# Kernel tuning notes

Hardware: AMD Instinct MI355X
Metric: run time of the kernel (lower is better)

The kernel has to match this reference:

```python
import jax, jax.numpy as jnp
import numpy as np
import math

B, L, C = 4096, 64, 256   # L == window_size
H = 8                     # num_heads
META_H = 384


def _rel_coords_log(W):
    # coords = meshgrid(arange(1), arange(W)) -> (2, W); first row is zeros
    c0 = jnp.zeros((W,), jnp.float32)
    c1 = jnp.arange(W, dtype=jnp.float32)
    coords = jnp.stack([c0, c1], axis=0)                      # (2, W)
    rel = coords[:, :, None] - coords[:, None, :]             # (2, W, W)
    rel = rel.transpose(1, 2, 0).reshape(-1, 2)               # (W*W, 2)
    return jnp.sign(rel) * jnp.log1p(jnp.abs(rel))


def setup_inputs() -> dict:
    key = jax.random.key(0)
    ks = jax.random.split(key, 8)
    s = 0.02
    return {
        "x": jax.random.normal(ks[0], (B, L, C), jnp.float32),
        "qkv_w": jax.random.normal(ks[1], (3 * C, C), jnp.float32) * s,
        "qkv_b": jnp.zeros((3 * C,), jnp.float32),
        "proj_w": jax.random.normal(ks[2], (C, C), jnp.float32) * s,
        "proj_b": jnp.zeros((C,), jnp.float32),
        "logit_scale": jnp.full((H,), math.log(10.0), jnp.float32),
        "mlp1_w": jax.random.normal(ks[3], (META_H, 2), jnp.float32) * s,
        "mlp1_b": jnp.zeros((META_H,), jnp.float32),
        "mlp2_w": jax.random.normal(ks[4], (H, META_H), jnp.float32) * s,
        "mlp2_b": jnp.zeros((H,), jnp.float32),
    }


def reference(x, qkv_w, qkv_b, proj_w, proj_b, logit_scale, mlp1_w, mlp1_b, mlp2_w, mlp2_b):
    b, l, c = x.shape
    h = H
    d = c // h
    qkv = x @ qkv_w.T + qkv_b                                 # (B, L, 3C)
    qkv = qkv.reshape(b, l, 3, h, d).transpose(2, 0, 3, 1, 4) # (3, B, H, L, D)
    q, k, v = qkv[0], qkv[1], qkv[2]
    # cosine attention: L2-normalize q, k (F.normalize, eps=1e-12)
    qn = q / jnp.maximum(jnp.linalg.norm(q, axis=-1, keepdims=True), 1e-12)
    kn = k / jnp.maximum(jnp.linalg.norm(k, axis=-1, keepdims=True), 1e-12)
    attn = jnp.einsum("bhld,bhmd->bhlm", qn, kn)              # (B, H, L, L)
    scale = jnp.exp(jnp.minimum(logit_scale, math.log(1.0 / 0.01)))
    attn = attn * scale.reshape(1, h, 1, 1)
    # MLP relative position bias
    rel = _rel_coords_log(l)                                  # (L*L, 2)
    hid = jax.nn.relu(rel @ mlp1_w.T + mlp1_b)                # (L*L, META_H)
    bias = (hid @ mlp2_w.T + mlp2_b).T.reshape(h, l, l)       # (H, L, L)
    attn = jax.nn.softmax(attn + bias[None], axis=-1)
    out = jnp.einsum("bhlm,bhmd->bhld", attn, v)              # (B, H, L, D)
    out = out.transpose(0, 2, 1, 3).reshape(b, l, c)
    return out @ proj_w.T + proj_b
```

## Files before the change

kernel.cpp:

```cpp
#include <hip/hip_runtime.h>
#include <hip/hip_bf16.h>

typedef __attribute__((ext_vector_type(4))) float f32x4;
typedef __attribute__((ext_vector_type(8))) short short8;
typedef __attribute__((ext_vector_type(4))) short short4_t;

#define LTOK 64
#define CDIM 256
#define FRS 576

static __device__ __forceinline__ short f2bf(float f) {
    __hip_bfloat16 h = __float2bfloat16(f);
    union { __hip_bfloat16 b; short s; } u; u.b = h;
    return u.s;
}
static __device__ __forceinline__ float bf2f(short s) {
    union { unsigned u; float f; } v;
    v.u = ((unsigned)(unsigned short)s) << 16;
    return v.f;
}
static __device__ __forceinline__ int KL(int l) { return l + (l >> 3); }

__global__ void prep_all(const float* __restrict__ qw, const float* __restrict__ pw,
                         const float* __restrict__ w1, const float* __restrict__ b1,
                         const float* __restrict__ w2, const float* __restrict__ b2,
                         const float* __restrict__ lsc,
                         short* __restrict__ wqs, short* __restrict__ wps,
                         float* __restrict__ biasT, float* __restrict__ scT) {
    if (blockIdx.x == 768) {
        int t = threadIdx.x;
        if (t < 8) scT[t] = expf(fminf(lsc[t], logf(100.0f)));
        if (t < 127) {
            float delta = (float)(t - 63);
            float sg = (delta > 0.f) ? 1.f : ((delta < 0.f) ? -1.f : 0.f);
            float r = sg * log1pf(fabsf(delta));
            float acc[8];
            #pragma unroll
            for (int q = 0; q < 8; ++q) acc[q] = b2[q];
            for (int m = 0; m < 384; ++m) {
                float hid = fmaxf(fmaf(r, w1[m * 2 + 1], b1[m]), 0.f);
                #pragma unroll
                for (int q = 0; q < 8; ++q) acc[q] = fmaf(hid, w2[q * 384 + m], acc[q]);
            }
            #pragma unroll
            for (int q = 0; q < 8; ++q) biasT[q * 127 + t] = acc[q];
        }
        return;
    }
    int i = blockIdx.x * 256 + threadIdx.x;
    {
        int row = i >> 8, col = i & 255;
        int nt = row >> 4, lcr = row & 15;
        int kt = col >> 5, lg = (col >> 3) & 3, j = col & 7;
        wqs[(size_t)(((nt * 8 + kt) * 64) + lg * 16 + lcr) * 8 + j] = f2bf(qw[i]);
    }
    if (i < 256 * 256) {
        int row = i >> 8, col = i & 255;
        int gs = row >> 4, lcr = row & 15;
        int h = col >> 5, lg = (col >> 3) & 3, j = col & 7;
        wps[(size_t)(((gs * 8 + h) * 64) + lg * 16 + lcr) * 8 + j] = f2bf(pw[i]);
    }
}


__global__ void __launch_bounds__(256, 5)
fused_win_attn(const float* __restrict__ x,
               const float* __restrict__ qkv_b,
               const short* __restrict__ wqs,
               const float* __restrict__ biasT,
               const float* __restrict__ scT,
               float* out)
{
    __shared__ short SH[13824];

    const int tid = threadIdx.x;
    const int w  = tid >> 6;
    const int l  = tid & 63;
    const int lg = l >> 4;
    const int lc = l & 15;
    const int li4 = lg * 4;
    const int blk = blockIdx.x;
    const int klb = KL(l) * 8;

    short* QGF = SH;
    short* KGF = SH + 4608;
    short* VTF = SH + 9216;

    short* ao = (short*)(out + (size_t)blk * (LTOK * CDIM) + 8192);

    short8 xf[8];
    {
        const float* xr = x + (size_t)blk * (LTOK * CDIM) + (size_t)(w * 16 + lc) * CDIM + lg * 8;
        #pragma unroll
        for (int kt = 0; kt < 8; ++kt) {
            f32x4 a = *(const f32x4*)(xr + kt * 32);
            f32x4 b = *(const f32x4*)(xr + kt * 32 + 4);
            short8 t;
            t[0]=f2bf(a[0]); t[1]=f2bf(a[1]); t[2]=f2bf(a[2]); t[3]=f2bf(a[3]);
            t[4]=f2bf(b[0]); t[5]=f2bf(b[1]); t[6]=f2bf(b[2]); t[7]=f2bf(b[3]);
            xf[kt] = t;
        }
    }
    const f32x4 fzero = {0.f, 0.f, 0.f, 0.f};
    short8 ones;
    #pragma unroll
    for (int j = 0; j < 8; ++j) ones[j] = (short)0x3F80;

    #pragma unroll 1
    for (int g = 0; g < 4; ++g) {
        #pragma unroll
        for (int sg = 0; sg < 6; ++sg) {
            const int st0 = sg * 2, st1 = sg * 2 + 1;
            const int gnt0 = (st0 >> 2) * 16 + g * 4 + (st0 & 3);
            const int gnt1 = (st1 >> 2) * 16 + g * 4 + (st1 & 3);
            const short* wb0 = wqs + ((size_t)(gnt0 * 8) * 64 + l) * 8;
            const short* wb1 = wqs + ((size_t)(gnt1 * 8) * 64 + l) * 8;
            f32x4 a0 = fzero, a1 = fzero;
            #pragma unroll
            for (int kt = 0; kt < 8; ++kt) {
                short8 Bf0 = *(const short8*)(wb0 + kt * 512);
                short8 Bf1 = *(const short8*)(wb1 + kt * 512);
                a0 = __builtin_amdgcn_mfma_f32_16x16x32_bf16(xf[kt], Bf0, a0, 0, 0, 0);
                a1 = __builtin_amdgcn_mfma_f32_16x16x32_bf16(xf[kt], Bf1, a1, 0, 0, 0);
            }
            #pragma unroll
            for (int e = 0; e < 2; ++e) {
                const int strip = e ? st1 : st0;
                const f32x4 av = e ? a1 : a0;
                const int s = strip >> 2, nt = strip & 3;
                const float bq = qkv_b[s * 256 + g * 64 + nt * 16 + lc];
                if (s < 2) {
                    short* base = (s ? KGF : QGF) + ((nt >> 1) * 4 + w) * FRS;
                    const int lgc = (nt & 1) * 2 + (lc >> 3);
                    #pragma unroll
                    for (int i = 0; i < 4; ++i) {
                        const int l2 = lgc * 16 + li4 + i;
                        base[KL(l2) * 8 + (lc & 7)] = f2bf(av[i] + bq);
                    }
                } else {
                    short* base = VTF + ((w >> 1) * 4 + nt) * FRS;
                    const int l2 = ((w & 1) * 2 + (lg >> 1)) * 16 + lc;
                    short4_t pk;
                    #pragma unroll
                    for (int i = 0; i < 4; ++i) pk[i] = f2bf(av[i] + bq);
                    *(short4_t*)(base + KL(l2) * 8 + (li4 & 7)) = pk;
                }
            }
        }
        __syncthreads();

        short8 Aq0 = *(const short8*)(QGF + (0 * 4 + w) * FRS + klb);
        short8 Aq1 = *(const short8*)(QGF + (1 * 4 + w) * FRS + klb);
        short* PW = QGF + w * FRS;

        #pragma unroll 1
        for (int hh = 0; hh < 2; ++hh) {
            const int h = 2 * g + hh;
            const float sc = scT[h];
            const short8 Aq = hh ? Aq1 : Aq0;
            float qn = 1e-24f;
            #pragma unroll
            for (int j = 0; j < 8; ++j) { float v = bf2f(Aq[j]); qn = fmaf(v, v, qn); }
            qn += __shfl_xor(qn, 16);
            qn += __shfl_xor(qn, 32);
            const float rq = rsqrtf(qn);
            f32x4 pacc[4];
            float invk[4];
            #pragma unroll
            for (int nt = 0; nt < 4; ++nt) {
                short8 Bk = *(const short8*)(KGF + (hh * 4 + nt) * FRS + klb);
                pacc[nt] = __builtin_amdgcn_mfma_f32_16x16x32_bf16(Aq, Bk, fzero, 0, 0, 0);
                float kn = 1e-24f;
                #pragma unroll
                for (int j = 0; j < 8; ++j) { float v = bf2f(Bk[j]); kn = fmaf(v, v, kn); }
                kn += __shfl_xor(kn, 16);
                kn += __shfl_xor(kn, 32);
                invk[nt] = rsqrtf(kn);
            }
            float iq[4];
            #pragma unroll
            for (int i = 0; i < 4; ++i) iq[i] = __shfl(rq, li4 + i, 16) * sc;
            const float* bt = biasT + h * 127 + w * 16 + 63 - lc;
            float p[4][4];
            #pragma unroll
            for (int i = 0; i < 4; ++i)
                #pragma unroll
                for (int nt = 0; nt < 4; ++nt)
                    p[i][nt] = __expf(pacc[nt][i] * iq[i] * invk[nt] + bt[li4 + i - nt * 16]);
            #pragma unroll
            for (int i = 0; i < 4; ++i)
                #pragma unroll
                for (int nt = 0; nt < 4; ++nt) {
                    const int l2 = ((nt & 1) * 2 + (lc >> 3)) * 16 + li4 + i;
                    PW[(nt >> 1) * 4 * FRS + KL(l2) * 8 + (lc & 7)] = f2bf(p[i][nt]);
                }
            f32x4 oacc[2], sacc;
            oacc[0] = fzero; oacc[1] = fzero; sacc = fzero;
            #pragma unroll
            for (int ktp = 0; ktp < 2; ++ktp) {
                short8 Ap = *(const short8*)(PW + ktp * 4 * FRS + klb);
                #pragma unroll
                for (int ndv = 0; ndv < 2; ++ndv) {
                    short8 Bv = *(const short8*)(VTF + (ktp * 4 + hh * 2 + ndv) * FRS + klb);
                    oacc[ndv] = __builtin_amdgcn_mfma_f32_16x16x32_bf16(Ap, Bv, oacc[ndv], 0, 0, 0);
                }
                sacc = __builtin_amdgcn_mfma_f32_16x16x32_bf16(Ap, ones, sacc, 0, 0, 0);
            }
            short8 aov;
            #pragma unroll
            for (int ndv = 0; ndv < 2; ++ndv)
                #pragma unroll
                for (int i = 0; i < 4; ++i)
                    aov[ndv * 4 + i] = f2bf(oacc[ndv][i] * (1.f / sacc[i]));
            *(short8*)(ao + ((size_t)((h * 4 + w) * 64 + l)) * 8) = aov;
        }
        __syncthreads();
    }
}

__global__ void __launch_bounds__(256, 4)
proj_win(const float* __restrict__ proj_b,
         const short* __restrict__ wps,
         float* out)
{
    __shared__ short AF[32 * FRS];

    const int tid = threadIdx.x;
    const int w  = tid >> 6;
    const int l  = tid & 63;
    const int lg = l >> 4;
    const int lc = l & 15;
    const int li4 = lg * 4;
    const int blk = blockIdx.x;
    const int klb = KL(l) * 8;

    const short* ao = (const short*)(out + (size_t)blk * (LTOK * CDIM) + 8192);

    #pragma unroll
    for (int u = 0; u < 8; ++u) {
        const int f = w * 8 + u;
        short8 t = *(const short8*)(ao + ((size_t)(f * 64 + l)) * 8);
        #pragma unroll
        for (int j = 0; j < 8; ++j) {
            const int r = lg * 4 + (j & 3);
            const int c = (j >> 2) * 16 + lc;
            AF[f * FRS + KL((c >> 3) * 16 + r) * 8 + (c & 7)] = t[j];
        }
    }
    __syncthreads();

    f32x4 accP[4][4];
    #pragma unroll
    for (int a = 0; a < 4; ++a)
        #pragma unroll
        for (int b = 0; b < 4; ++b) accP[a][b] = (f32x4){0,0,0,0};

    #pragma unroll
    for (int kt = 0; kt < 8; ++kt) {
        short8 Aa0 = *(const short8*)(AF + (kt * 4 + 0) * FRS + klb);
        short8 Aa1 = *(const short8*)(AF + (kt * 4 + 1) * FRS + klb);
        short8 Aa2 = *(const short8*)(AF + (kt * 4 + 2) * FRS + klb);
        short8 Aa3 = *(const short8*)(AF + (kt * 4 + 3) * FRS + klb);
        #pragma unroll
        for (int ntl = 0; ntl < 4; ++ntl) {
            short8 Bp = *(const short8*)(wps + ((size_t)((w * 4 + ntl) * 8 + kt) * 64 + l) * 8);
            accP[0][ntl] = __builtin_amdgcn_mfma_f32_16x16x32_bf16(Aa0, Bp, accP[0][ntl], 0, 0, 0);
            accP[1][ntl] = __builtin_amdgcn_mfma_f32_16x16x32_bf16(Aa1, Bp, accP[1][ntl], 0, 0, 0);
            accP[2][ntl] = __builtin_amdgcn_mfma_f32_16x16x32_bf16(Aa2, Bp, accP[2][ntl], 0, 0, 0);
            accP[3][ntl] = __builtin_amdgcn_mfma_f32_16x16x32_bf16(Aa3, Bp, accP[3][ntl], 0, 0, 0);
        }
    }

    float* ob = out + (size_t)blk * (LTOK * CDIM);
    #pragma unroll
    for (int ntl = 0; ntl < 4; ++ntl) {
        const float pb = proj_b[w * 64 + ntl * 16 + lc];
        #pragma unroll
        for (int mt = 0; mt < 4; ++mt)
            #pragma unroll
            for (int i = 0; i < 4; ++i)
                ob[(size_t)(mt * 16 + li4 + i) * 256 + w * 64 + ntl * 16 + lc] = accP[mt][ntl][i] + pb;
    }
}

extern "C" void kernel_launch(void* const* d_in, const int* in_sizes, int n_in,
                              void* d_out, int out_size, void* d_ws, size_t ws_size,
                              hipStream_t stream) {
    const float* x     = (const float*)d_in[0];
    const float* qkvw  = (const float*)d_in[1];
    const float* qkvb  = (const float*)d_in[2];
    const float* projw = (const float*)d_in[3];
    const float* projb = (const float*)d_in[4];
    const float* lsc   = (const float*)d_in[5];
    const float* w1    = (const float*)d_in[6];
    const float* b1    = (const float*)d_in[7];
    const float* w2    = (const float*)d_in[8];
    const float* b2    = (const float*)d_in[9];
    float* out = (float*)d_out;

    short* wqs   = (short*)d_ws;
    short* wps   = (short*)((char*)d_ws + 393216);
    float* biasT = (float*)((char*)d_ws + 524288);
    float* scT   = (float*)((char*)d_ws + 528384);

    const int nwin = in_sizes[0] / (LTOK * CDIM);

    prep_all<<<769, 256, 0, stream>>>(qkvw, projw, w1, b1, w2, b2, lsc, wqs, wps, biasT, scT);
    fused_win_attn<<<nwin, 256, 0, stream>>>(x, qkvb, wqs, biasT, scT, out);
    proj_win<<<nwin, 256, 0, stream>>>(projb, wps, out);
}
```

Measured before the change: 505.2 us.

## Interleave two heads' QK phase and halve proj LDS for higher occupancy

In the attention kernel the per-head loop is unrolled. Both heads' norms and QK MFMAs are issued together, which raises instruction-level parallelism but holds more registers. The projection kernel now stages the attention output into LDS in two halves using half the shared memory, with an extra barrier, and raises launch bounds from 4 to 5 blocks per CU. This trades an extra sync and register pressure for more resident blocks.

```diff
diff --git a/kernel.cpp b/kernel.cpp
--- a/kernel.cpp
+++ b/kernel.cpp
@@ -153,40 +153,50 @@
         short8 Aq1 = *(const short8*)(QGF + (1 * 4 + w) * FRS + klb);
         short* PW = QGF + w * FRS;
 
-        #pragma unroll 1
-        for (int hh = 0; hh < 2; ++hh) {
-            const int h = 2 * g + hh;
-            const float sc = scT[h];
-            const short8 Aq = hh ? Aq1 : Aq0;
-            float qn = 1e-24f;
-            #pragma unroll
-            for (int j = 0; j < 8; ++j) { float v = bf2f(Aq[j]); qn = fmaf(v, v, qn); }
-            qn += __shfl_xor(qn, 16);
-            qn += __shfl_xor(qn, 32);
-            const float rq = rsqrtf(qn);
-            f32x4 pacc[4];
-            float invk[4];
-            #pragma unroll
-            for (int nt = 0; nt < 4; ++nt) {
-                short8 Bk = *(const short8*)(KGF + (hh * 4 + nt) * FRS + klb);
-                pacc[nt] = __builtin_amdgcn_mfma_f32_16x16x32_bf16(Aq, Bk, fzero, 0, 0, 0);
-                float kn = 1e-24f;
-                #pragma unroll
-                for (int j = 0; j < 8; ++j) { float v = bf2f(Bk[j]); kn = fmaf(v, v, kn); }
-                kn += __shfl_xor(kn, 16);
-                kn += __shfl_xor(kn, 32);
-                invk[nt] = rsqrtf(kn);
-            }
-            float iq[4];
-            #pragma unroll
-            for (int i = 0; i < 4; ++i) iq[i] = __shfl(rq, li4 + i, 16) * sc;
-            const float* bt = biasT + h * 127 + w * 16 + 63 - lc;
+        float qn0 = 1e-24f, qn1 = 1e-24f;
+        #pragma unroll
+        for (int j = 0; j < 8; ++j) {
+            float v0 = bf2f(Aq0[j]); qn0 = fmaf(v0, v0, qn0);
+            float v1 = bf2f(Aq1[j]); qn1 = fmaf(v1, v1, qn1);
+        }
+        qn0 += __shfl_xor(qn0, 16); qn1 += __shfl_xor(qn1, 16);
+        qn0 += __shfl_xor(qn0, 32); qn1 += __shfl_xor(qn1, 32);
+        const float rq0 = rsqrtf(qn0), rq1 = rsqrtf(qn1);
+        const float sc0 = scT[2 * g], sc1 = scT[2 * g + 1];
+        float iq0[4], iq1[4];
+        #pragma unroll
+        for (int i = 0; i < 4; ++i) {
+            iq0[i] = __shfl(rq0, li4 + i, 16) * sc0;
+            iq1[i] = __shfl(rq1, li4 + i, 16) * sc1;
+        }
+        f32x4 pacc0[4], pacc1[4];
+        float invk0[4], invk1[4];
+        #pragma unroll
+        for (int nt = 0; nt < 4; ++nt) {
+            short8 Bk0 = *(const short8*)(KGF + nt * FRS + klb);
+            short8 Bk1 = *(const short8*)(KGF + (4 + nt) * FRS + klb);
+            pacc0[nt] = __builtin_amdgcn_mfma_f32_16x16x32_bf16(Aq0, Bk0, fzero, 0, 0, 0);
+            pacc1[nt] = __builtin_amdgcn_mfma_f32_16x16x32_bf16(Aq1, Bk1, fzero, 0, 0, 0);
+            float kn0 = 1e-24f, kn1 = 1e-24f;
+            #pragma unroll
+            for (int j = 0; j < 8; ++j) {
+                float v0 = bf2f(Bk0[j]); kn0 = fmaf(v0, v0, kn0);
+                float v1 = bf2f(Bk1[j]); kn1 = fmaf(v1, v1, kn1);
+            }
+            kn0 += __shfl_xor(kn0, 16); kn1 += __shfl_xor(kn1, 16);
+            kn0 += __shfl_xor(kn0, 32); kn1 += __shfl_xor(kn1, 32);
+            invk0[nt] = rsqrtf(kn0);
+            invk1[nt] = rsqrtf(kn1);
+        }
+
+        {
+            const float* bt = biasT + (2 * g) * 127 + w * 16 + 63 - lc;
             float p[4][4];
             #pragma unroll
             for (int i = 0; i < 4; ++i)
                 #pragma unroll
                 for (int nt = 0; nt < 4; ++nt)
-                    p[i][nt] = __expf(pacc[nt][i] * iq[i] * invk[nt] + bt[li4 + i - nt * 16]);
+                    p[i][nt] = __expf(pacc0[nt][i] * iq0[i] * invk0[nt] + bt[li4 + i - nt * 16]);
             #pragma unroll
             for (int i = 0; i < 4; ++i)
                 #pragma unroll
@@ -201,7 +211,7 @@
                 short8 Ap = *(const short8*)(PW + ktp * 4 * FRS + klb);
                 #pragma unroll
                 for (int ndv = 0; ndv < 2; ++ndv) {
-                    short8 Bv = *(const short8*)(VTF + (ktp * 4 + hh * 2 + ndv) * FRS + klb);
+                    short8 Bv = *(const short8*)(VTF + (ktp * 4 + ndv) * FRS + klb);
                     oacc[ndv] = __builtin_amdgcn_mfma_f32_16x16x32_bf16(Ap, Bv, oacc[ndv], 0, 0, 0);
                 }
                 sacc = __builtin_amdgcn_mfma_f32_16x16x32_bf16(Ap, ones, sacc, 0, 0, 0);
@@ -212,18 +222,53 @@
                 #pragma unroll
                 for (int i = 0; i < 4; ++i)
                     aov[ndv * 4 + i] = f2bf(oacc[ndv][i] * (1.f / sacc[i]));
-            *(short8*)(ao + ((size_t)((h * 4 + w) * 64 + l)) * 8) = aov;
+            *(short8*)(ao + ((size_t)(((2 * g) * 4 + w) * 64 + l)) * 8) = aov;
+        }
+        {
+            const float* bt = biasT + (2 * g + 1) * 127 + w * 16 + 63 - lc;
+            float p[4][4];
+            #pragma unroll
+            for (int i = 0; i < 4; ++i)
+                #pragma unroll
+                for (int nt = 0; nt < 4; ++nt)
+                    p[i][nt] = __expf(pacc1[nt][i] * iq1[i] * invk1[nt] + bt[li4 + i - nt * 16]);
+            #pragma unroll
+            for (int i = 0; i < 4; ++i)
+                #pragma unroll
+                for (int nt = 0; nt < 4; ++nt) {
+                    const int l2 = ((nt & 1) * 2 + (lc >> 3)) * 16 + li4 + i;
+                    PW[(nt >> 1) * 4 * FRS + KL(l2) * 8 + (lc & 7)] = f2bf(p[i][nt]);
+                }
+            f32x4 oacc[2], sacc;
+            oacc[0] = fzero; oacc[1] = fzero; sacc = fzero;
+            #pragma unroll
+            for (int ktp = 0; ktp < 2; ++ktp) {
+                short8 Ap = *(const short8*)(PW + ktp * 4 * FRS + klb);
+                #pragma unroll
+                for (int ndv = 0; ndv < 2; ++ndv) {
+                    short8 Bv = *(const short8*)(VTF + (ktp * 4 + 2 + ndv) * FRS + klb);
+                    oacc[ndv] = __builtin_amdgcn_mfma_f32_16x16x32_bf16(Ap, Bv, oacc[ndv], 0, 0, 0);
+                }
+                sacc = __builtin_amdgcn_mfma_f32_16x16x32_bf16(Ap, ones, sacc, 0, 0, 0);
+            }
+            short8 aov;
+            #pragma unroll
+            for (int ndv = 0; ndv < 2; ++ndv)
+                #pragma unroll
+                for (int i = 0; i < 4; ++i)
+                    aov[ndv * 4 + i] = f2bf(oacc[ndv][i] * (1.f / sacc[i]));
+            *(short8*)(ao + ((size_t)(((2 * g + 1) * 4 + w) * 64 + l)) * 8) = aov;
         }
         __syncthreads();
     }
 }
 
-__global__ void __launch_bounds__(256, 4)
+__global__ void __launch_bounds__(256, 5)
 proj_win(const float* __restrict__ proj_b,
          const short* __restrict__ wps,
          float* out)
 {
-    __shared__ short AF[32 * FRS];
+    __shared__ short AF[16 * FRS];
 
     const int tid = threadIdx.x;
     const int w  = tid >> 6;
@@ -236,19 +281,6 @@
 
     const short* ao = (const short*)(out + (size_t)blk * (LTOK * CDIM) + 8192);
 
-    #pragma unroll
-    for (int u = 0; u < 8; ++u) {
-        const int f = w * 8 + u;
-        short8 t = *(const short8*)(ao + ((size_t)(f * 64 + l)) * 8);
-        #pragma unroll
-        for (int j = 0; j < 8; ++j) {
-            const int r = lg * 4 + (j & 3);
-            const int c = (j >> 2) * 16 + lc;
-            AF[f * FRS + KL((c >> 3) * 16 + r) * 8 + (c & 7)] = t[j];
-        }
-    }
-    __syncthreads();
-
     f32x4 accP[4][4];
     #pragma unroll
     for (int a = 0; a < 4; ++a)
@@ -256,18 +288,35 @@
         for (int b = 0; b < 4; ++b) accP[a][b] = (f32x4){0,0,0,0};
 
     #pragma unroll
-    for (int kt = 0; kt < 8; ++kt) {
-        short8 Aa0 = *(const short8*)(AF + (kt * 4 + 0) * FRS + klb);
-        short8 Aa1 = *(const short8*)(AF + (kt * 4 + 1) * FRS + klb);
-        short8 Aa2 = *(const short8*)(AF + (kt * 4 + 2) * FRS + klb);
-        short8 Aa3 = *(const short8*)(AF + (kt * 4 + 3) * FRS + klb);
-        #pragma unroll
-        for (int ntl = 0; ntl < 4; ++ntl) {
-            short8 Bp = *(const short8*)(wps + ((size_t)((w * 4 + ntl) * 8 + kt) * 64 + l) * 8);
-            accP[0][ntl] = __builtin_amdgcn_mfma_f32_16x16x32_bf16(Aa0, Bp, accP[0][ntl], 0, 0, 0);
-            accP[1][ntl] = __builtin_amdgcn_mfma_f32_16x16x32_bf16(Aa1, Bp, accP[1][ntl], 0, 0, 0);
-            accP[2][ntl] = __builtin_amdgcn_mfma_f32_16x16x32_bf16(Aa2, Bp, accP[2][ntl], 0, 0, 0);
-            accP[3][ntl] = __builtin_amdgcn_mfma_f32_16x16x32_bf16(Aa3, Bp, accP[3][ntl], 0, 0, 0);
+    for (int ph = 0; ph < 2; ++ph) {
+        if (ph) __syncthreads();
+        #pragma unroll
+        for (int u = 0; u < 4; ++u) {
+            const int fl = w * 4 + u;
+            short8 t = *(const short8*)(ao + ((size_t)((ph * 16 + fl) * 64 + l)) * 8);
+            #pragma unroll
+            for (int j = 0; j < 8; ++j) {
+                const int r = lg * 4 + (j & 3);
+                const int c = (j >> 2) * 16 + lc;
+                AF[fl * FRS + KL((c >> 3) * 16 + r) * 8 + (c & 7)] = t[j];
+            }
+        }
+        __syncthreads();
+        #pragma unroll
+        for (int kt2 = 0; kt2 < 4; ++kt2) {
+            short8 Aa0 = *(const short8*)(AF + (kt2 * 4 + 0) * FRS + klb);
+            short8 Aa1 = *(const short8*)(AF + (kt2 * 4 + 1) * FRS + klb);
+            short8 Aa2 = *(const short8*)(AF + (kt2 * 4 + 2) * FRS + klb);
+            short8 Aa3 = *(const short8*)(AF + (kt2 * 4 + 3) * FRS + klb);
+            const int kt = ph * 4 + kt2;
+            #pragma unroll
+            for (int ntl = 0; ntl < 4; ++ntl) {
+                short8 Bp = *(const short8*)(wps + ((size_t)((w * 4 + ntl) * 8 + kt) * 64 + l) * 8);
+                accP[0][ntl] = __builtin_amdgcn_mfma_f32_16x16x32_bf16(Aa0, Bp, accP[0][ntl], 0, 0, 0);
+                accP[1][ntl] = __builtin_amdgcn_mfma_f32_16x16x32_bf16(Aa1, Bp, accP[1][ntl], 0, 0, 0);
+                accP[2][ntl] = __builtin_amdgcn_mfma_f32_16x16x32_bf16(Aa2, Bp, accP[2][ntl], 0, 0, 0);
+                accP[3][ntl] = __builtin_amdgcn_mfma_f32_16x16x32_bf16(Aa3, Bp, accP[3][ntl], 0, 0, 0);
+            }
         }
     }
 
```

Result: slower. 807.4 us (+59.8%).
